# Kernel tuning notes

Measured on AMD Instinct MI355X. Metric: run time of the kernel, lower is better.

The kernel has to match this reference:

```python
import jax, jax.numpy as jnp
import numpy as np

T, D_IN, D, H, A = 8192, 2048, 512, 512, 18  # seq_len, obs_dim, dense_size, cell_size, action_size


def setup_inputs() -> dict:
    key = jax.random.key(0)
    ks = jax.random.split(key, 12)
    g = lambda k, sh, s: (jax.random.normal(k, sh, jnp.float32) * s)
    return {
        "x": g(ks[0], (T, D_IN), 1.0),
        "prev_hidden": jnp.zeros((1, H), jnp.float32),
        "W1": g(ks[1], (D_IN, D), 0.02), "b1": jnp.zeros((D,), jnp.float32),
        "W2": g(ks[2], (D, D), 0.04),    "b2": jnp.zeros((D,), jnp.float32),
        "Wg": g(ks[3], (D, 3 * H), 0.04),   # GRU input kernel [D, 3H] (z|r|h)
        "Ug": g(ks[4], (H, 3 * H), 0.04),   # GRU recurrent kernel [H, 3H]
        "bg": jnp.zeros((2, 3 * H), jnp.float32),  # reset_after=True: input + recurrent bias
        "Wp": g(ks[5], (H, A), 0.05), "bp": jnp.zeros((A,), jnp.float32),
        "Wv": g(ks[6], (H, 1), 0.05), "bv": jnp.zeros((1,), jnp.float32),
    }


def reference(x, prev_hidden, W1, b1, W2, b2, Wg, Ug, bg, Wp, bp, Wv, bv):
    # MLP front-end (relu)
    z = jax.nn.relu(x @ W1 + b1)
    z = jax.nn.relu(z @ W2 + b2)
    # Precompute input projections for all timesteps: [T, 3H]
    X = z @ Wg + bg[0]
    b_rec = bg[1]

    def step(h, xt):  # h: [1,H], xt: [3H]
        rec = h @ Ug + b_rec                    # [1, 3H]
        xz, xr, xh = jnp.split(xt, 3)           # each [H]
        rz, rr, rh = jnp.split(rec, 3, axis=1)  # each [1, H]
        zt = jax.nn.sigmoid(xz + rz)
        rt = jax.nn.sigmoid(xr + rr)
        hh = jax.nn.sigmoid(xh + rt * rh)       # activation='sigmoid' (candidate)
        hn = zt * h + (1.0 - zt) * hh
        return hn, hn[0]

    hT, seq = jax.lax.scan(step, prev_hidden, X)  # seq: [T, H]
    policy = jax.nn.softmax(seq @ Wp + bp, axis=-1)
    value = seq @ Wv + bv
    return policy, value, hT
```

## Files before the change

### kernel.cpp

```cpp
#include <hip/hip_runtime.h>
#include <hip/hip_bf16.h>


#define T_STEPS 8192
#define DIN 2048
#define DD 512
#define HHH 512
#define AACT 18
#define H3 1536
#define NWG 32

typedef __attribute__((ext_vector_type(8))) short short8;
typedef __attribute__((ext_vector_type(4))) float f32x4;

__global__ void cast_f32_bf16(const float* __restrict__ in,
                              __hip_bfloat16* __restrict__ out, int n)
{
    int i = blockIdx.x * 256 + threadIdx.x;
    if (i < n) out[i] = __float2bfloat16(in[i]);
}

__global__ __launch_bounds__(256) void gemm_bf16(
    const float* __restrict__ A32, const __hip_bfloat16* __restrict__ A16,
    const __hip_bfloat16* __restrict__ B, const float* __restrict__ bias,
    __hip_bfloat16* __restrict__ Cb, float* __restrict__ Cf,
    int M, int N, int K, int relu)
{
    const int m0 = blockIdx.x * 64;
    const int n0 = blockIdx.y * 64;
    const int t  = threadIdx.x;
    const int wave = t >> 6;
    const int lane = t & 63;
    const int quad = lane >> 4;
    const int l16  = lane & 15;

    __shared__ __align__(16) __hip_bfloat16 As[64 * 40];
    __shared__ __align__(16) __hip_bfloat16 Bs[64 * 40];

    f32x4 acc[4];
#pragma unroll
    for (int c = 0; c < 4; ++c) acc[c] = (f32x4){0.f, 0.f, 0.f, 0.f};

    const int ar = t >> 2, akc = (t & 3) * 8;
    const int bk = t >> 3, bn  = (t & 7) * 8;

    for (int kb = 0; kb < K; kb += 32) {
        if (A32) {
            const float* src = A32 + (size_t)(m0 + ar) * K + kb + akc;
            float4 f0 = *(const float4*)(src);
            float4 f1 = *(const float4*)(src + 4);
            union { short8 v; __hip_bfloat16 h[8]; } u;
            u.h[0] = __float2bfloat16(f0.x); u.h[1] = __float2bfloat16(f0.y);
            u.h[2] = __float2bfloat16(f0.z); u.h[3] = __float2bfloat16(f0.w);
            u.h[4] = __float2bfloat16(f1.x); u.h[5] = __float2bfloat16(f1.y);
            u.h[6] = __float2bfloat16(f1.z); u.h[7] = __float2bfloat16(f1.w);
            *(short8*)&As[ar * 40 + akc] = u.v;
        } else {
            const __hip_bfloat16* src = A16 + (size_t)(m0 + ar) * K + kb + akc;
            *(short8*)&As[ar * 40 + akc] = *(const short8*)src;
        }
        {
            const __hip_bfloat16* src = B + (size_t)(kb + bk) * N + n0 + bn;
            short8 v = *(const short8*)src;
            const __hip_bfloat16* vh = (const __hip_bfloat16*)&v;
#pragma unroll
            for (int i = 0; i < 8; ++i) Bs[(bn + i) * 40 + bk] = vh[i];
        }
        __syncthreads();

        short8 a = *(const short8*)&As[(wave * 16 + l16) * 40 + quad * 8];
#pragma unroll
        for (int c = 0; c < 4; ++c) {
            short8 b = *(const short8*)&Bs[(c * 16 + l16) * 40 + quad * 8];
            acc[c] = __builtin_amdgcn_mfma_f32_16x16x32_bf16(a, b, acc[c], 0, 0, 0);
        }
        __syncthreads();
    }

#pragma unroll
    for (int c = 0; c < 4; ++c) {
        const int col = n0 + c * 16 + l16;
        const float bb = bias ? bias[col] : 0.f;
#pragma unroll
        for (int r = 0; r < 4; ++r) {
            const int row = m0 + wave * 16 + quad * 4 + r;
            float v = acc[c][r] + bb;
            if (relu) v = fmaxf(v, 0.f);
            if (Cb) Cb[(size_t)row * N + col] = __float2bfloat16(v);
            if (Cf) Cf[(size_t)row * N + col] = v;
        }
    }
}

__global__ __launch_bounds__(256)
__attribute__((amdgpu_waves_per_eu(1, 1)))
void scan_kernel(
    const float* __restrict__ X,
    const float* __restrict__ Ug,
    const float* __restrict__ bg,
    const float* __restrict__ h0,
    float* __restrict__ seq,
    unsigned long long* __restrict__ hbuf,
    float* __restrict__ hT)
{
    const int t  = threadIdx.x;
    const int wg = blockIdx.x;
    const int jl = t >> 4;
    const int kp = t & 15;
    const int j  = wg * 16 + jl;
    const int k0 = kp * 32;

    __shared__ __align__(16) float h_lds[2][16 * 36];

    float wz[32], wr[32], wh[32];
#pragma unroll
    for (int m = 0; m < 32; ++m) {
        const float* row = Ug + (size_t)(k0 + m) * H3;
        wz[m] = row[j];
        wr[m] = row[512 + j];
        wh[m] = row[1024 + j];
    }
#pragma unroll
    for (int m = 0; m < 32; ++m) {
        asm volatile("" : "+a"(wz[m]), "+a"(wr[m]), "+a"(wh[m]));
    }

    const float* brec = bg + H3;
    const float bz = brec[j], brr = brec[512 + j], bh = brec[1024 + j];
    float hj = h0[j];

    const int k1 = t, k2 = t + 256;
    const int a1 = (k1 >> 5) * 36 + (k1 & 31);
    const int a2 = (k2 >> 5) * 36 + (k2 & 31);

    float xz = 0.f, xr = 0.f, xh = 0.f;
    if (kp == 0) { xz = X[j]; xr = X[512 + j]; xh = X[1024 + j]; }

    for (int s = 0; s < T_STEPS; ++s) {
        float* hl = h_lds[s & 1];

        if (s == 0) {
            hl[a1] = h0[k1];
            hl[a2] = h0[k2];
        } else {
            const unsigned long long* src = hbuf + (size_t)(s & 1) * 512;
            unsigned long long v1 = __hip_atomic_load(src + k1, __ATOMIC_RELAXED, __HIP_MEMORY_SCOPE_AGENT);
            unsigned long long v2 = __hip_atomic_load(src + k2, __ATOMIC_RELAXED, __HIP_MEMORY_SCOPE_AGENT);
            bool ok1 = (unsigned)(v1 >> 32) == (unsigned)s;
            bool ok2 = (unsigned)(v2 >> 32) == (unsigned)s;
            while (!(ok1 && ok2)) {
                if (!ok1) v1 = __hip_atomic_load(src + k1, __ATOMIC_RELAXED, __HIP_MEMORY_SCOPE_AGENT);
                if (!ok2) v2 = __hip_atomic_load(src + k2, __ATOMIC_RELAXED, __HIP_MEMORY_SCOPE_AGENT);
                ok1 = (unsigned)(v1 >> 32) == (unsigned)s;
                ok2 = (unsigned)(v2 >> 32) == (unsigned)s;
            }
            hl[a1] = __uint_as_float((unsigned)v1);
            hl[a2] = __uint_as_float((unsigned)v2);
        }
        __syncthreads();

        float nxz = 0.f, nxr = 0.f, nxh = 0.f;
        if (kp == 0 && s + 1 < T_STEPS) {
            const float* Xs = X + (size_t)(s + 1) * H3;
            nxz = Xs[j]; nxr = Xs[512 + j]; nxh = Xs[1024 + j];
        }

        float accz = 0.f, accr = 0.f, acch = 0.f;
        const float* hb = &hl[kp * 36];
#pragma unroll
        for (int m = 0; m < 32; m += 4) {
            float4 hv = *(const float4*)(hb + m);
            accz = fmaf(hv.x, wz[m    ], accz);
            accz = fmaf(hv.y, wz[m + 1], accz);
            accz = fmaf(hv.z, wz[m + 2], accz);
            accz = fmaf(hv.w, wz[m + 3], accz);
            accr = fmaf(hv.x, wr[m    ], accr);
            accr = fmaf(hv.y, wr[m + 1], accr);
            accr = fmaf(hv.z, wr[m + 2], accr);
            accr = fmaf(hv.w, wr[m + 3], accr);
            acch = fmaf(hv.x, wh[m    ], acch);
            acch = fmaf(hv.y, wh[m + 1], acch);
            acch = fmaf(hv.z, wh[m + 2], acch);
            acch = fmaf(hv.w, wh[m + 3], acch);
        }
#pragma unroll
        for (int off = 8; off; off >>= 1) {
            accz += __shfl_down(accz, off, 16);
            accr += __shfl_down(accr, off, 16);
            acch += __shfl_down(acch, off, 16);
        }

        if (kp == 0) {
            const float rz = accz + bz, rr = accr + brr, rh = acch + bh;
            const float zt = 1.f / (1.f + __expf(-(xz + rz)));
            const float rt = 1.f / (1.f + __expf(-(xr + rr)));
            const float hc = 1.f / (1.f + __expf(-(xh + rt * rh)));
            const float hn = zt * hj + (1.f - zt) * hc;
            hj = hn;
            unsigned long long pk =
                ((unsigned long long)(unsigned)(s + 1) << 32) | (unsigned)__float_as_uint(hn);
            __hip_atomic_store(hbuf + (size_t)((s + 1) & 1) * 512 + j, pk,
                               __ATOMIC_RELAXED, __HIP_MEMORY_SCOPE_AGENT);
            seq[(size_t)s * HHH + j] = hn;
            if (s == T_STEPS - 1) hT[j] = hn;
        }
        xz = nxz; xr = nxr; xh = nxh;
    }
}

__global__ __launch_bounds__(64) void heads_kernel(
    const float* __restrict__ seq, const float* __restrict__ Wp,
    const float* __restrict__ bp, const float* __restrict__ Wv,
    const float* __restrict__ bv, float* __restrict__ pol,
    float* __restrict__ val)
{
    const int s = blockIdx.x;
    const int l = threadIdx.x;
    const float* h = seq + (size_t)s * HHH;

    float acc[19];
#pragma unroll
    for (int jj = 0; jj < 19; ++jj) acc[jj] = 0.f;

#pragma unroll
    for (int kk = 0; kk < 8; ++kk) {
        const int k = kk * 64 + l;
        const float hv = h[k];
        const float* wrow = Wp + (size_t)k * AACT;
#pragma unroll
        for (int jj = 0; jj < AACT; ++jj) acc[jj] = fmaf(hv, wrow[jj], acc[jj]);
        acc[18] = fmaf(hv, Wv[k], acc[18]);
    }
#pragma unroll
    for (int jj = 0; jj < 19; ++jj) {
        float v = acc[jj];
#pragma unroll
        for (int off = 32; off; off >>= 1) v += __shfl_down(v, off, 64);
        acc[jj] = v;
    }
    if (l == 0) {
        float lg[18], mx = -1e30f;
#pragma unroll
        for (int jj = 0; jj < AACT; ++jj) { lg[jj] = acc[jj] + bp[jj]; mx = fmaxf(mx, lg[jj]); }
        float sum = 0.f;
#pragma unroll
        for (int jj = 0; jj < AACT; ++jj) { lg[jj] = __expf(lg[jj] - mx); sum += lg[jj]; }
        const float inv = 1.f / sum;
#pragma unroll
        for (int jj = 0; jj < AACT; ++jj) pol[(size_t)s * AACT + jj] = lg[jj] * inv;
        val[s] = acc[18] + bv[0];
    }
}

extern "C" void kernel_launch(void* const* d_in, const int* in_sizes, int n_in,
                              void* d_out, int out_size, void* d_ws, size_t ws_size,
                              hipStream_t stream)
{
    const float* x  = (const float*)d_in[0];
    const float* h0 = (const float*)d_in[1];
    const float* W1 = (const float*)d_in[2];
    const float* b1 = (const float*)d_in[3];
    const float* W2 = (const float*)d_in[4];
    const float* b2 = (const float*)d_in[5];
    const float* Wg = (const float*)d_in[6];
    const float* Ug = (const float*)d_in[7];
    const float* bg = (const float*)d_in[8];
    const float* Wp = (const float*)d_in[9];
    const float* bp = (const float*)d_in[10];
    const float* Wv = (const float*)d_in[11];
    const float* bv = (const float*)d_in[12];

    char* ws = (char*)d_ws;
    __hip_bfloat16* W1b = (__hip_bfloat16*)(ws + 0);
    __hip_bfloat16* W2b = (__hip_bfloat16*)(ws + 2097152);
    __hip_bfloat16* Wgb = (__hip_bfloat16*)(ws + 2621440);
    __hip_bfloat16* z1b = (__hip_bfloat16*)(ws + 4194304);
    __hip_bfloat16* z2b = (__hip_bfloat16*)(ws + 12582912);
    float*          Xb  = (float*)(ws + 20971520);
    float*          seq = (float*)(ws + 71303168);
    unsigned long long* hbuf = (unsigned long long*)(ws + 88080384);

    float* out = (float*)d_out;
    float* pol = out;
    float* val = out + (size_t)T_STEPS * AACT;
    float* hT  = out + (size_t)T_STEPS * AACT + T_STEPS;

    cast_f32_bf16<<<DIN * DD / 256, 256, 0, stream>>>(W1, W1b, DIN * DD);
    cast_f32_bf16<<<DD * DD / 256, 256, 0, stream>>>(W2, W2b, DD * DD);
    cast_f32_bf16<<<DD * H3 / 256, 256, 0, stream>>>(Wg, Wgb, DD * H3);

    dim3 blk(256);
    gemm_bf16<<<dim3(T_STEPS / 64, DD / 64), blk, 0, stream>>>(
        x, nullptr, W1b, b1, z1b, nullptr, T_STEPS, DD, DIN, 1);
    gemm_bf16<<<dim3(T_STEPS / 64, DD / 64), blk, 0, stream>>>(
        nullptr, z1b, W2b, b2, z2b, nullptr, T_STEPS, DD, DD, 1);
    gemm_bf16<<<dim3(T_STEPS / 64, H3 / 64), blk, 0, stream>>>(
        nullptr, z2b, Wgb, bg, nullptr, Xb, T_STEPS, H3, DD, 0);

    scan_kernel<<<NWG, 256, 0, stream>>>(Xb, Ug, bg, h0, seq, hbuf, hT);

    heads_kernel<<<T_STEPS, 64, 0, stream>>>(seq, Wp, bp, Wv, bv, pol, val);
}
```

Measured before the change: 12.94 ms.

## Pack hidden-state exchange into 16-byte flagged slots with DPP reductions

Each thread in the recurrent scan now polls a single 16-byte slot holding two hidden values, each with its own step tag, using system-coherent dwordx4 loads instead of two 8-byte atomic loads. Producers pair adjacent outputs via a shuffle and publish them with one dwordx4 store. This halves the number of polling loads per thread on the per-step critical path. The shuffle-down reduction becomes DPP row-shift adds, and the next-step X prefetch is moved ahead of the wait. A spin guard with a global abort flag is added to avoid deadlock, at the cost of an extra init kernel and a check after every barrier. The abort path can exit early and leave the output incomplete.

```diff
diff --git a/kernel.cpp b/kernel.cpp
--- a/kernel.cpp
+++ b/kernel.cpp
@@ -12,6 +12,7 @@
 
 typedef __attribute__((ext_vector_type(8))) short short8;
 typedef __attribute__((ext_vector_type(4))) float f32x4;
+typedef __attribute__((ext_vector_type(4))) int i32x4;
 
 __global__ void cast_f32_bf16(const float* __restrict__ in,
                               __hip_bfloat16* __restrict__ out, int n)
@@ -19,6 +20,8 @@
     int i = blockIdx.x * 256 + threadIdx.x;
     if (i < n) out[i] = __float2bfloat16(in[i]);
 }
+
+__global__ void init_ctl(int* ctl) { ctl[0] = 0; ctl[1] = 0; ctl[2] = 0; }
 
 __global__ __launch_bounds__(256) void gemm_bf16(
     const float* __restrict__ A32, const __hip_bfloat16* __restrict__ A16,
@@ -92,6 +95,13 @@
     }
 }
 
+template <int CTRL>
+__device__ __forceinline__ float dpp_red_add(float x)
+{
+    int sh = __builtin_amdgcn_update_dpp(0, __float_as_int(x), CTRL, 0xF, 0xF, true);
+    return x + __int_as_float(sh);
+}
+
 __global__ __launch_bounds__(256)
 __attribute__((amdgpu_waves_per_eu(1, 1)))
 void scan_kernel(
@@ -100,8 +110,9 @@
     const float* __restrict__ bg,
     const float* __restrict__ h0,
     float* __restrict__ seq,
-    unsigned long long* __restrict__ hbuf,
-    float* __restrict__ hT)
+    i32x4* __restrict__ hbuf,
+    float* __restrict__ hT,
+    int* __restrict__ ctl)
 {
     const int t  = threadIdx.x;
     const int wg = blockIdx.x;
@@ -111,6 +122,8 @@
     const int k0 = kp * 32;
 
     __shared__ __align__(16) float h_lds[2][16 * 36];
+    __shared__ int wg_abort;
+    if (t == 0) wg_abort = 0;
 
     float wz[32], wr[32], wh[32];
 #pragma unroll
@@ -129,41 +142,47 @@
     const float bz = brec[j], brr = brec[512 + j], bh = brec[1024 + j];
     float hj = h0[j];
 
-    const int k1 = t, k2 = t + 256;
-    const int a1 = (k1 >> 5) * 36 + (k1 & 31);
-    const int a2 = (k2 >> 5) * 36 + (k2 & 31);
+    const int a_e = jl * 36 + 2 * kp;
 
     float xz = 0.f, xr = 0.f, xh = 0.f;
     if (kp == 0) { xz = X[j]; xr = X[512 + j]; xh = X[1024 + j]; }
 
     for (int s = 0; s < T_STEPS; ++s) {
         float* hl = h_lds[s & 1];
-
-        if (s == 0) {
-            hl[a1] = h0[k1];
-            hl[a2] = h0[k2];
-        } else {
-            const unsigned long long* src = hbuf + (size_t)(s & 1) * 512;
-            unsigned long long v1 = __hip_atomic_load(src + k1, __ATOMIC_RELAXED, __HIP_MEMORY_SCOPE_AGENT);
-            unsigned long long v2 = __hip_atomic_load(src + k2, __ATOMIC_RELAXED, __HIP_MEMORY_SCOPE_AGENT);
-            bool ok1 = (unsigned)(v1 >> 32) == (unsigned)s;
-            bool ok2 = (unsigned)(v2 >> 32) == (unsigned)s;
-            while (!(ok1 && ok2)) {
-                if (!ok1) v1 = __hip_atomic_load(src + k1, __ATOMIC_RELAXED, __HIP_MEMORY_SCOPE_AGENT);
-                if (!ok2) v2 = __hip_atomic_load(src + k2, __ATOMIC_RELAXED, __HIP_MEMORY_SCOPE_AGENT);
-                ok1 = (unsigned)(v1 >> 32) == (unsigned)s;
-                ok2 = (unsigned)(v2 >> 32) == (unsigned)s;
-            }
-            hl[a1] = __uint_as_float((unsigned)v1);
-            hl[a2] = __uint_as_float((unsigned)v2);
-        }
-        __syncthreads();
 
         float nxz = 0.f, nxr = 0.f, nxh = 0.f;
         if (kp == 0 && s + 1 < T_STEPS) {
             const float* Xs = X + (size_t)(s + 1) * H3;
             nxz = Xs[j]; nxr = Xs[512 + j]; nxh = Xs[1024 + j];
         }
+
+        if (s == 0) {
+            *(float2*)&hl[a_e] = make_float2(h0[2 * t], h0[2 * t + 1]);
+        } else {
+            const i32x4* sp = hbuf + ((s & 1) << 8) + t;
+            i32x4 d;
+            int guard = 0;
+            for (;;) {
+                asm volatile("global_load_dwordx4 %0, %1, off sc0 sc1\n\t"
+                             "s_waitcnt vmcnt(0)"
+                             : "=v"(d) : "v"(sp) : "memory");
+                if (__builtin_expect(d[1] == s && d[3] == s, 1)) break;
+                if ((++guard & 255) == 0) {
+                    int ab = __hip_atomic_load(ctl + 2, __ATOMIC_RELAXED,
+                                               __HIP_MEMORY_SCOPE_AGENT);
+                    if (ab || guard > (1 << 14)) {
+                        wg_abort = 1;
+                        __hip_atomic_store(ctl + 2, 1, __ATOMIC_RELAXED,
+                                           __HIP_MEMORY_SCOPE_AGENT);
+                        break;
+                    }
+                }
+            }
+            *(float2*)&hl[a_e] =
+                make_float2(__int_as_float(d[0]), __int_as_float(d[2]));
+        }
+        __syncthreads();
+        if (wg_abort) return;
 
         float accz = 0.f, accr = 0.f, acch = 0.f;
         const float* hb = &hl[kp * 36];
@@ -183,12 +202,18 @@
             acch = fmaf(hv.z, wh[m + 2], acch);
             acch = fmaf(hv.w, wh[m + 3], acch);
         }
-#pragma unroll
-        for (int off = 8; off; off >>= 1) {
-            accz += __shfl_down(accz, off, 16);
-            accr += __shfl_down(accr, off, 16);
-            acch += __shfl_down(acch, off, 16);
-        }
+        accz = dpp_red_add<0x108>(accz);
+        accr = dpp_red_add<0x108>(accr);
+        acch = dpp_red_add<0x108>(acch);
+        accz = dpp_red_add<0x104>(accz);
+        accr = dpp_red_add<0x104>(accr);
+        acch = dpp_red_add<0x104>(acch);
+        accz = dpp_red_add<0x102>(accz);
+        accr = dpp_red_add<0x102>(accr);
+        acch = dpp_red_add<0x102>(acch);
+        accz = dpp_red_add<0x101>(accz);
+        accr = dpp_red_add<0x101>(accr);
+        acch = dpp_red_add<0x101>(acch);
 
         if (kp == 0) {
             const float rz = accz + bz, rr = accr + brr, rh = acch + bh;
@@ -197,11 +222,16 @@
             const float hc = 1.f / (1.f + __expf(-(xh + rt * rh)));
             const float hn = zt * hj + (1.f - zt) * hc;
             hj = hn;
-            unsigned long long pk =
-                ((unsigned long long)(unsigned)(s + 1) << 32) | (unsigned)__float_as_uint(hn);
-            __hip_atomic_store(hbuf + (size_t)((s + 1) & 1) * 512 + j, pk,
-                               __ATOMIC_RELAXED, __HIP_MEMORY_SCOPE_AGENT);
-            seq[(size_t)s * HHH + j] = hn;
+            const float ho = __shfl_down(hn, 16, 64);
+            if ((t & 31) == 0) {
+                i32x4 pk;
+                pk[0] = __float_as_int(hn); pk[1] = s + 1;
+                pk[2] = __float_as_int(ho); pk[3] = s + 1;
+                i32x4* dst = hbuf + (((s + 1) & 1) << 8) + (wg * 8 + (jl >> 1));
+                asm volatile("global_store_dwordx4 %0, %1, off sc0 sc1"
+                             :: "v"(dst), "v"(pk) : "memory");
+                *(float2*)&seq[(size_t)s * HHH + j] = make_float2(hn, ho);
+            }
             if (s == T_STEPS - 1) hT[j] = hn;
         }
         xz = nxz; xr = nxr; xh = nxh;
@@ -278,7 +308,8 @@
     __hip_bfloat16* z2b = (__hip_bfloat16*)(ws + 12582912);
     float*          Xb  = (float*)(ws + 20971520);
     float*          seq = (float*)(ws + 71303168);
-    unsigned long long* hbuf = (unsigned long long*)(ws + 88080384);
+    i32x4*          hbuf = (i32x4*)(ws + 88080384);
+    int* ctl = (int*)(ws + 4194304);
 
     float* out = (float*)d_out;
     float* pol = out;
@@ -297,7 +328,8 @@
     gemm_bf16<<<dim3(T_STEPS / 64, H3 / 64), blk, 0, stream>>>(
         nullptr, z2b, Wgb, bg, nullptr, Xb, T_STEPS, H3, DD, 0);
 
-    scan_kernel<<<NWG, 256, 0, stream>>>(Xb, Ug, bg, h0, seq, hbuf, hT);
+    init_ctl<<<1, 1, 0, stream>>>(ctl);
+    scan_kernel<<<NWG, 256, 0, stream>>>(Xb, Ug, bg, h0, seq, hbuf, hT, ctl);
 
     heads_kernel<<<T_STEPS, 64, 0, stream>>>(seq, Wp, bp, Wv, bv, pol, val);
 }
```

New measurement: 12.98 ms. No clear change (+0.3%).
